# Kernel optimization log

Measured on AMD Instinct MI355X. Metric: run time of the kernel, lower is better.

## Reference

```python
import jax, jax.numpy as jnp
import numpy as np

B, N, F_IN, F_OUT, H = 8, 1024, 128, 64, 4
EPS = 1e-7
NEG_SLOPE = 0.2


def setup_inputs() -> dict:
    key = jax.random.key(0)
    k_a, k_x, k_w, k_aw, k_ab = jax.random.split(key, 5)
    A = jax.random.randint(k_a, (B, N, N), 0, 2).astype(jnp.float32)
    x = jax.random.normal(k_x, (B, N, F_IN), dtype=jnp.float32)
    # per-head params (stacked over head axis): GAT.W (xavier-normal-ish), attention Linear(2F->1)
    W = jax.random.normal(k_w, (H, F_IN, F_OUT), dtype=jnp.float32) * np.sqrt(2.0 / (F_IN + F_OUT))
    lim = 1.0 / np.sqrt(2 * F_OUT)
    a_w = jax.random.uniform(k_aw, (H, 2 * F_OUT), minval=-lim, maxval=lim, dtype=jnp.float32)
    a_b = jax.random.uniform(k_ab, (H,), minval=-lim, maxval=lim, dtype=jnp.float32)
    return {"A": A, "x": x, "W": W, "a_w": a_w, "a_b": a_b}


def reference(A, x, W, a_w, a_b):
    # Wh: (B, H, N, F_OUT)
    Wh = jnp.einsum('bnf,hfo->bhno', x, W)
    # attention linear on concat([Wh_i, Wh_j]) is separable: a1.Wh_i + a2.Wh_j + b
    a1, a2 = a_w[:, :F_OUT], a_w[:, F_OUT:]
    s_i = jnp.einsum('bhno,ho->bhn', Wh, a1)   # depends on row index i (dim 1 of (B,N,N))
    s_j = jnp.einsum('bhno,ho->bhn', Wh, a2)   # depends on col index j (dim 2)
    e = s_i[:, :, :, None] + s_j[:, :, None, :] + a_b[None, :, None, None]  # (B,H,Ni,Nj)
    e = jnp.where(e >= 0, e, NEG_SLOPE * e)  # LeakyReLU(0.2)
    # masked softmax as in source: exp, mask by A, normalize over dim=1 of (B,N,N) -> axis 2 here
    exps = jnp.exp(e) * A[:, None, :, :]
    attn = exps / (jnp.sum(exps, axis=2, keepdims=True) + EPS)
    out = jnp.einsum('bhij,bhjo->bhio', attn, Wh)  # matmul over j
    # concat heads on feature dim: (B, N, H*F_OUT)
    return out.transpose(0, 2, 1, 3).reshape(B, N, H * F_OUT)
```

## Files before the change

kernel.cpp:

```cpp
#include <hip/hip_runtime.h>
#include <hip/hip_bf16.h>
#include <hip/hip_fp16.h>

#define BB 8
#define NN 1024
#define FIN 128
#define FOUT 64
#define HH 4
#define EPSV 1e-7f
#define SLOPE 0.2f
#define LOG2E 1.44269504088896340736f

typedef _Float16 v8h __attribute__((ext_vector_type(8)));
typedef _Float16 v4h __attribute__((ext_vector_type(4)));
typedef _Float16 v2h __attribute__((ext_vector_type(2)));
typedef __fp16 v2hf __attribute__((ext_vector_type(2)));
typedef float v4f __attribute__((ext_vector_type(4)));

union U8 { v2h p[4]; v8h v; };
union U2 { v2hf hf; v2h h; };

__device__ __forceinline__ v2h clamp01(v2h x) {
  v2h zero = {(_Float16)0.0f, (_Float16)0.0f};
  v2h one = {(_Float16)1.0f, (_Float16)1.0f};
  return __builtin_elementwise_min(__builtin_elementwise_max(x, zero), one);
}

__device__ __forceinline__ v2h cvt2(float a, float b) {
  U2 u;
  u.hf = __builtin_amdgcn_cvt_pkrtz(a, b);
  return u.h;
}

__device__ __forceinline__ float dot2(v2h a, v2h b, float c) {
  U2 ua, ub;
  ua.h = a;
  ub.h = b;
  return __builtin_amdgcn_fdot2(ua.hf, ub.hf, c, false);
}

__global__ __launch_bounds__(256) void k0_wt(const float* __restrict__ W,
                                             _Float16* __restrict__ Wtt) {
  for (int it = 0; it < 16; ++it) {
    int idx = blockIdx.x * 4096 + it * 256 + threadIdx.x;
    int e = idx & 7, ln = (idx >> 3) & 15, kgg = (idx >> 7) & 15,
        ct = idx >> 11;
    int c = ct * 16 + ln, k = kgg * 8 + e;
    Wtt[idx] = (_Float16)W[(size_t)(c >> 6) * 8192 + k * 64 + (c & 63)];
  }
}

__global__ __launch_bounds__(256) void k1_whm(
    const float* __restrict__ x, const _Float16* __restrict__ Wtt,
    const float* __restrict__ aw, const float* __restrict__ ab,
    _Float16* __restrict__ WhTt, float* __restrict__ si2,
    _Float16* __restrict__ tjh, _Float16* __restrict__ djh,
    _Float16* __restrict__ e2jh, float* __restrict__ e2i_t,
    float* __restrict__ di_t, float* __restrict__ colsum) {
  __shared__ _Float16 xs[16][136];
  int tid = threadIdx.x;
  int bid = blockIdx.x;
  if (tid < 64) colsum[bid * 64 + tid] = 0.0f;
#pragma unroll
  for (int t2 = 0; t2 < 2; ++t2) {
    int idx = t2 * 256 + tid;
    int row = idx >> 5, c4 = (idx & 31) * 4;
    float4 v = *(const float4*)(x + ((size_t)bid * 16 + row) * FIN + c4);
    v4h hv;
    hv[0] = (_Float16)v.x; hv[1] = (_Float16)v.y;
    hv[2] = (_Float16)v.z; hv[3] = (_Float16)v.w;
    *(v4h*)(&xs[row][c4]) = hv;
  }
  __syncthreads();
  int w = tid >> 6, l = tid & 63;
  int kg = l >> 4, ln = l & 15;
  v4f acc[4] = {{}, {}, {}, {}};
#pragma unroll
  for (int ks = 0; ks < 4; ++ks) {
    v8h af = *(const v8h*)(&xs[ln][ks * 32 + kg * 8]);
    int kgg = ks * 4 + kg;
#pragma unroll
    for (int t = 0; t < 4; ++t) {
      int ct = w * 4 + t;
      v8h bf = *(const v8h*)(Wtt + (((size_t)ct * 16 + kgg) * 16 + ln) * 8);
      acc[t] = __builtin_amdgcn_mfma_f32_16x16x32_f16(af, bf, acc[t], 0, 0, 0);
    }
  }
  float a1v[4], a2v[4];
#pragma unroll
  for (int t = 0; t < 4; ++t) {
    a1v[t] = aw[w * 128 + t * 16 + ln];
    a2v[t] = aw[w * 128 + 64 + t * 16 + ln];
  }
  float abv = ab[w];
#pragma unroll
  for (int r = 0; r < 4; ++r) {
    float v1 = acc[0][r] * a1v[0] + acc[1][r] * a1v[1] +
               acc[2][r] * a1v[2] + acc[3][r] * a1v[3];
    float v2 = acc[0][r] * a2v[0] + acc[1][r] * a2v[1] +
               acc[2][r] * a2v[2] + acc[3][r] * a2v[3];
#pragma unroll
    for (int off = 1; off < 16; off <<= 1) {
      v1 += __shfl_xor(v1, off);
      v2 += __shfl_xor(v2, off);
    }
    if (ln == 0) {
      int gr = bid * 16 + kg * 4 + r;
      int b_ = gr >> 10, n_ = gr & 1023;
      size_t row = ((size_t)b_ * HH + w) * NN + n_;
      float v1L = v1 * LOG2E;
      float tjL = (v2 + abv) * LOG2E;
      si2[row] = v1L;
      float e1i = __builtin_amdgcn_exp2f(v1L);
      float e2i = __builtin_amdgcn_exp2f(0.2f * v1L);
      e2i_t[row] = e2i;
      di_t[row] = e1i - e2i;
      float e1j = __builtin_amdgcn_exp2f(tjL);
      float e2j = __builtin_amdgcn_exp2f(0.2f * tjL);
      tjh[row] = (_Float16)tjL;
      e2jh[row] = (_Float16)e2j;
      djh[row] = (_Float16)(e1j - e2j);
    }
  }
  {
    int b_ = bid >> 6;
    int bh = b_ * HH + w;
    int jb = (bid & 63) >> 1;
    int jj0 = (bid & 1) * 16 + kg * 4;
#pragma unroll
    for (int t = 0; t < 4; ++t) {
      v4h hv;
#pragma unroll
      for (int r = 0; r < 4; ++r) hv[r] = (_Float16)acc[t][r];
      *(v4h*)(WhTt + (((size_t)bh * 32 + jb) * 64 + (t * 16 + ln)) * 32 +
              jj0) = hv;
    }
  }
}

__global__ __launch_bounds__(256) void kb_colsum_bits(
    const float* __restrict__ A, const float* __restrict__ si2,
    const float* __restrict__ e2i_t, const float* __restrict__ di_t,
    const _Float16* __restrict__ tjh, const _Float16* __restrict__ djh,
    const _Float16* __restrict__ e2jh, float* __restrict__ colsum,
    unsigned long long* __restrict__ Abits) {
  __shared__ v2h si_p[4][16], di_p[4][16], e2i_p[4][16];
  int b = blockIdx.z, is = blockIdx.y, jt = blockIdx.x;
  int tid = threadIdx.x;
  int w = tid >> 6, lane = tid & 63;
  int j = jt * 256 + tid;
  int i0 = is * 32;
  if (tid < 64) {
    int h = tid >> 4, pp = tid & 15;
    size_t row = ((size_t)(b * HH + h)) * NN + i0 + 2 * pp;
    si_p[h][pp] = cvt2(si2[row], si2[row + 1]);
    di_p[h][pp] = cvt2(di_t[row], di_t[row + 1]);
    e2i_p[h][pp] = cvt2(e2i_t[row], e2i_t[row + 1]);
  }
  __syncthreads();
  v2h tjb[4], djb[4], ejb[4];
#pragma unroll
  for (int h = 0; h < 4; ++h) {
    size_t jr = ((size_t)(b * HH + h)) * NN + j;
    _Float16 t = tjh[jr], d = djh[jr], e = e2jh[jr];
    tjb[h][0] = t; tjb[h][1] = t;
    djb[h][0] = d; djb[h][1] = d;
    ejb[h][0] = e; ejb[h][1] = e;
  }
  v2h big = {(_Float16)4096.0f, (_Float16)4096.0f};
  float acc[4] = {0.f, 0.f, 0.f, 0.f};
  const float* Ap = A + ((size_t)b * NN + i0) * NN + j;
  unsigned long long myword = 0ull;
#pragma unroll
  for (int c = 0; c < 4; ++c) {
    float av[8];
#pragma unroll
    for (int q = 0; q < 8; ++q) av[q] = Ap[(size_t)(c * 8 + q) * NN];
    v2h apk[4];
#pragma unroll
    for (int q = 0; q < 4; ++q) apk[q] = cvt2(av[2 * q], av[2 * q + 1]);
#pragma unroll
    for (int q = 0; q < 8; ++q) {
      unsigned long long m = __ballot(av[q] != 0.0f);
      if (lane == c * 8 + q) myword = m;
    }
#pragma unroll
    for (int h = 0; h < 4; ++h) {
      U8 si4, di4, ei4;
      si4.v = *(const v8h*)&si_p[h][c * 4];
      di4.v = *(const v8h*)&di_p[h][c * 4];
      ei4.v = *(const v8h*)&e2i_p[h][c * 4];
#pragma unroll
      for (int pp = 0; pp < 4; ++pp) {
        v2h f = si4.p[pp] + tjb[h];
        v2h s = clamp01(f * big);
        v2h ei = s * di4.p[pp] + ei4.p[pp];
        v2h ej = s * djb[h] + ejb[h];
        v2h p = ei * ej;
        acc[h] = dot2(p, apk[pp], acc[h]);
      }
    }
  }
  if (lane < 32)
    Abits[((size_t)b * NN + i0 + lane) * 16 + jt * 4 + w] = myword;
#pragma unroll
  for (int h = 0; h < 4; ++h)
    atomicAdd(&colsum[((size_t)(b * HH + h)) * NN + j], acc[h]);
}

__global__ __launch_bounds__(512, 4) void k4_pv(
    const unsigned long long* __restrict__ Abits,
    const float* __restrict__ si2, const _Float16* __restrict__ tjh,
    const _Float16* __restrict__ djh, const _Float16* __restrict__ e2jh,
    const float* __restrict__ e2i_t, const float* __restrict__ di_t,
    const _Float16* __restrict__ WhTt, const float* __restrict__ colsum,
    float* __restrict__ out) {
  __shared__ unsigned long long Ab[64][17];
  __shared__ _Float16 tjl[2][1024];
  __shared__ _Float16 djl[2][1024];
  __shared__ _Float16 e2jl[2][1024];
  __shared__ _Float16 lut[256][8];
  __shared__ float sil[2][64], e2il[2][64], dil[2][64];
  __shared__ float red[2][2][64][33];
  int bid = blockIdx.x;
  int b = bid & 7, hp = (bid >> 3) & 1, it = bid >> 4;
  int i0 = it * 64;
  int tid = threadIdx.x;
  {
    size_t base = (size_t)(b * HH + hp * 2) * NN;
#pragma unroll
    for (int t2 = 0; t2 < 4; ++t2) {
      int idx = t2 * 512 + tid;
      int hh = idx >> 10, j = idx & 1023;
      size_t row = base + (size_t)hh * NN + j;
      float rr = 1.0f / (colsum[row] + EPSV);
      tjl[hh][j] = tjh[row];
      djl[hh][j] = (_Float16)((float)djh[row] * rr);
      e2jl[hh][j] = (_Float16)((float)e2jh[row] * rr);
    }
  }
  if (tid < 128) {
    int hh = tid >> 6, ii = tid & 63;
    size_t row = (size_t)(b * HH + hp * 2 + hh) * NN + i0 + ii;
    sil[hh][ii] = si2[row];
    e2il[hh][ii] = e2i_t[row];
    dil[hh][ii] = di_t[row];
  }
  if (tid < 256) {
#pragma unroll
    for (int e = 0; e < 8; ++e)
      lut[tid][e] = ((tid >> e) & 1) ? (_Float16)1.0f : (_Float16)0.0f;
  }
  {
#pragma unroll
    for (int t2 = 0; t2 < 2; ++t2) {
      int idx = t2 * 512 + tid;
      int row = idx >> 4, word = idx & 15;
      Ab[row][word] = Abits[((size_t)b * NN + i0 + row) * 16 + word];
    }
  }
  __syncthreads();

  int w = tid >> 6, l = tid & 63;
  int hh = w & 1, jq4 = w >> 1;
  int kg = l >> 4, ln = l & 15;
  v2h si_f[4], e2_f[4], di_f[4];
#pragma unroll
  for (int f = 0; f < 4; ++f) {
    _Float16 s = (_Float16)sil[hh][f * 16 + ln];
    _Float16 e = (_Float16)e2il[hh][f * 16 + ln];
    _Float16 d = (_Float16)dil[hh][f * 16 + ln];
    si_f[f][0] = s; si_f[f][1] = s;
    e2_f[f][0] = e; e2_f[f][1] = e;
    di_f[f][0] = d; di_f[f][1] = d;
  }
  v2h big = {(_Float16)4096.0f, (_Float16)4096.0f};
  int bh = b * HH + hp * 2 + hh;
  v4f acc[4][4] = {};
  const _Float16* VTb = WhTt + (size_t)bh * 32 * 64 * 32;
  int jbase = jq4 * 256;

  for (int jq = 0; jq < 8; ++jq) {
    int j = jbase + jq * 32 + kg * 8;
    int widx = j >> 6, sh = j & 63;
    U8 tj8, dj8, ej8;
    tj8.v = *(const v8h*)&tjl[hh][j];
    dj8.v = *(const v8h*)&djl[hh][j];
    ej8.v = *(const v8h*)&e2jl[hh][j];
    const _Float16* vb = VTb + (size_t)(j >> 5) * 2048 + kg * 8;
    v8h b0 = *(const v8h*)(vb + (0 * 16 + ln) * 32);
    v8h b1 = *(const v8h*)(vb + (1 * 16 + ln) * 32);
    v8h b2 = *(const v8h*)(vb + (2 * 16 + ln) * 32);
    v8h b3 = *(const v8h*)(vb + (3 * 16 + ln) * 32);
#pragma unroll
    for (int f = 0; f < 4; ++f) {
      unsigned int bits = (unsigned int)(Ab[f * 16 + ln][widx] >> sh) & 0xffu;
      U8 m, af;
      m.v = *(const v8h*)&lut[bits][0];
#pragma unroll
      for (int q = 0; q < 4; ++q) {
        v2h fv = tj8.p[q] + si_f[f];
        v2h s = clamp01(fv * big);
        v2h ej = s * dj8.p[q] + ej8.p[q];
        v2h ei = s * di_f[f] + e2_f[f];
        af.p[q] = ei * ej * m.p[q];
      }
      acc[f][0] =
          __builtin_amdgcn_mfma_f32_16x16x32_f16(af.v, b0, acc[f][0], 0, 0, 0);
      acc[f][1] =
          __builtin_amdgcn_mfma_f32_16x16x32_f16(af.v, b1, acc[f][1], 0, 0, 0);
      acc[f][2] =
          __builtin_amdgcn_mfma_f32_16x16x32_f16(af.v, b2, acc[f][2], 0, 0, 0);
      acc[f][3] =
          __builtin_amdgcn_mfma_f32_16x16x32_f16(af.v, b3, acc[f][3], 0, 0, 0);
    }
  }

#pragma unroll
  for (int pass = 0; pass < 2; ++pass) {
    int fA = pass * 2, fB = pass * 2 + 1;
    if (pass) __syncthreads();
    if (jq4 == 1 || jq4 == 3) {
      int slot = jq4 >> 1;
#pragma unroll
      for (int t = 0; t < 4; ++t)
#pragma unroll
        for (int r = 0; r < 4; ++r) {
          red[hh][slot][l][t * 4 + r] = acc[fA][t][r];
          red[hh][slot][l][16 + t * 4 + r] = acc[fB][t][r];
        }
    }
    __syncthreads();
    if (jq4 == 0 || jq4 == 2) {
      int slot = jq4 >> 1;
#pragma unroll
      for (int t = 0; t < 4; ++t)
#pragma unroll
        for (int r = 0; r < 4; ++r) {
          acc[fA][t][r] += red[hh][slot][l][t * 4 + r];
          acc[fB][t][r] += red[hh][slot][l][16 + t * 4 + r];
        }
    }
    __syncthreads();
    if (jq4 == 2) {
#pragma unroll
      for (int t = 0; t < 4; ++t)
#pragma unroll
        for (int r = 0; r < 4; ++r) {
          red[hh][0][l][t * 4 + r] = acc[fA][t][r];
          red[hh][0][l][16 + t * 4 + r] = acc[fB][t][r];
        }
    }
    __syncthreads();
    if (jq4 == 0) {
#pragma unroll
      for (int t = 0; t < 4; ++t)
#pragma unroll
        for (int r = 0; r < 4; ++r) {
          acc[fA][t][r] += red[hh][0][l][t * 4 + r];
          acc[fB][t][r] += red[hh][0][l][16 + t * 4 + r];
        }
#pragma unroll
      for (int r = 0; r < 4; ++r) {
        int giA = i0 + fA * 16 + kg * 4 + r;
        float* opA = out + ((size_t)b * NN + giA) * 256 + (hp * 2 + hh) * 64;
        opA[0 * 16 + ln] = acc[fA][0][r];
        opA[1 * 16 + ln] = acc[fA][1][r];
        opA[2 * 16 + ln] = acc[fA][2][r];
        opA[3 * 16 + ln] = acc[fA][3][r];
        float* opB = opA + 16 * 256;
        opB[0 * 16 + ln] = acc[fB][0][r];
        opB[1 * 16 + ln] = acc[fB][1][r];
        opB[2 * 16 + ln] = acc[fB][2][r];
        opB[3 * 16 + ln] = acc[fB][3][r];
      }
    }
  }
}

extern "C" void kernel_launch(void* const* d_in, const int* in_sizes, int n_in,
                              void* d_out, int out_size, void* d_ws,
                              size_t ws_size, hipStream_t stream) {
  const float* A = (const float*)d_in[0];
  const float* x = (const float*)d_in[1];
  const float* W = (const float*)d_in[2];
  const float* aw = (const float*)d_in[3];
  const float* ab = (const float*)d_in[4];
  float* out = (float*)d_out;
  char* ws = (char*)d_ws;
  _Float16* WhTt = (_Float16*)ws;
  _Float16* Wtt = (_Float16*)(ws + (4u << 20));
  float* si2 = (float*)(ws + (4u << 20) + (64u << 10));
  float* colsum = (float*)(ws + (4u << 20) + (192u << 10));
  unsigned long long* Abits =
      (unsigned long long*)(ws + (4u << 20) + (320u << 10));
  char* tb = ws + (5u << 20) + (320u << 10);
  _Float16* tjh = (_Float16*)tb;
  _Float16* djh = (_Float16*)(tb + (64u << 10));
  _Float16* e2jh = (_Float16*)(tb + (128u << 10));
  float* e2i_t = (float*)(tb + (192u << 10));
  float* di_t = (float*)(tb + (320u << 10));

  hipLaunchKernelGGL(k0_wt, dim3(8), dim3(256), 0, stream, W, Wtt);
  hipLaunchKernelGGL(k1_whm, dim3(512), dim3(256), 0, stream, x, Wtt, aw, ab,
                     WhTt, si2, tjh, djh, e2jh, e2i_t, di_t, colsum);
  hipLaunchKernelGGL(kb_colsum_bits, dim3(4, 32, BB), dim3(256), 0, stream, A,
                     si2, e2i_t, di_t, tjh, djh, e2jh, colsum, Abits);
  hipLaunchKernelGGL(k4_pv, dim3(256), dim3(512), 0, stream, Abits, si2, tjh,
                     djh, e2jh, e2i_t, di_t, WhTt, colsum, out);
}
```

Measured before the change: 41.20 us.

## Fuse weight transpose into projection kernel via per-block LDS staging

Removes the separate k0_wt kernel that converted W to fp16 in an MFMA-tiled layout. Each k1_whm block now loads all of W in fp32, converts it, and scatters it into a 64KB shared-memory buffer. The MFMA B fragments are then read from LDS instead of global memory. This saves one kernel launch and its global round trip. In exchange, all 512 blocks each re-read the full W from cache, do scattered LDS writes, and need about 68KB of LDS per block, which lowers occupancy.

```diff
diff --git a/kernel.cpp b/kernel.cpp
--- a/kernel.cpp
+++ b/kernel.cpp
@@ -39,28 +39,33 @@
   return __builtin_amdgcn_fdot2(ua.hf, ub.hf, c, false);
 }
 
-__global__ __launch_bounds__(256) void k0_wt(const float* __restrict__ W,
-                                             _Float16* __restrict__ Wtt) {
-  for (int it = 0; it < 16; ++it) {
-    int idx = blockIdx.x * 4096 + it * 256 + threadIdx.x;
-    int e = idx & 7, ln = (idx >> 3) & 15, kgg = (idx >> 7) & 15,
-        ct = idx >> 11;
-    int c = ct * 16 + ln, k = kgg * 8 + e;
-    Wtt[idx] = (_Float16)W[(size_t)(c >> 6) * 8192 + k * 64 + (c & 63)];
-  }
-}
-
 __global__ __launch_bounds__(256) void k1_whm(
-    const float* __restrict__ x, const _Float16* __restrict__ Wtt,
+    const float* __restrict__ x, const float* __restrict__ W,
     const float* __restrict__ aw, const float* __restrict__ ab,
     _Float16* __restrict__ WhTt, float* __restrict__ si2,
     _Float16* __restrict__ tjh, _Float16* __restrict__ djh,
     _Float16* __restrict__ e2jh, float* __restrict__ e2i_t,
     float* __restrict__ di_t, float* __restrict__ colsum) {
+  __shared__ _Float16 wlds[32768];
   __shared__ _Float16 xs[16][136];
   int tid = threadIdx.x;
   int bid = blockIdx.x;
   if (tid < 64) colsum[bid * 64 + tid] = 0.0f;
+#pragma unroll 4
+  for (int it = 0; it < 32; ++it) {
+    int idx4 = it * 256 + tid;
+    int base = idx4 * 4;
+    int h = base >> 13, k = (base >> 6) & 127, o0 = base & 63;
+    float4 v = *(const float4*)(W + (size_t)h * 8192 + k * 64 + o0);
+    int kgg = k >> 3, e = k & 7;
+#pragma unroll
+    for (int q = 0; q < 4; ++q) {
+      int c = h * 64 + o0 + q;
+      int ct = c >> 4, ln = c & 15;
+      float val = (q == 0) ? v.x : (q == 1) ? v.y : (q == 2) ? v.z : v.w;
+      wlds[(((ct * 16) + kgg) * 16 + ln) * 8 + e] = (_Float16)val;
+    }
+  }
 #pragma unroll
   for (int t2 = 0; t2 < 2; ++t2) {
     int idx = t2 * 256 + tid;
@@ -82,7 +87,7 @@
 #pragma unroll
     for (int t = 0; t < 4; ++t) {
       int ct = w * 4 + t;
-      v8h bf = *(const v8h*)(Wtt + (((size_t)ct * 16 + kgg) * 16 + ln) * 8);
+      v8h bf = *(const v8h*)(&wlds[(((ct * 16) + kgg) * 16 + ln) * 8]);
       acc[t] = __builtin_amdgcn_mfma_f32_16x16x32_f16(af, bf, acc[t], 0, 0, 0);
     }
   }
@@ -389,20 +394,18 @@
   float* out = (float*)d_out;
   char* ws = (char*)d_ws;
   _Float16* WhTt = (_Float16*)ws;
-  _Float16* Wtt = (_Float16*)(ws + (4u << 20));
-  float* si2 = (float*)(ws + (4u << 20) + (64u << 10));
-  float* colsum = (float*)(ws + (4u << 20) + (192u << 10));
+  float* si2 = (float*)(ws + (4u << 20));
+  float* colsum = (float*)(ws + (4u << 20) + (128u << 10));
   unsigned long long* Abits =
-      (unsigned long long*)(ws + (4u << 20) + (320u << 10));
-  char* tb = ws + (5u << 20) + (320u << 10);
+      (unsigned long long*)(ws + (4u << 20) + (256u << 10));
+  char* tb = ws + (5u << 20) + (256u << 10);
   _Float16* tjh = (_Float16*)tb;
   _Float16* djh = (_Float16*)(tb + (64u << 10));
   _Float16* e2jh = (_Float16*)(tb + (128u << 10));
   float* e2i_t = (float*)(tb + (192u << 10));
   float* di_t = (float*)(tb + (320u << 10));
 
-  hipLaunchKernelGGL(k0_wt, dim3(8), dim3(256), 0, stream, W, Wtt);
-  hipLaunchKernelGGL(k1_whm, dim3(512), dim3(256), 0, stream, x, Wtt, aw, ab,
+  hipLaunchKernelGGL(k1_whm, dim3(512), dim3(256), 0, stream, x, W, aw, ab,
                      WhTt, si2, tjh, djh, e2jh, e2i_t, di_t, colsum);
   hipLaunchKernelGGL(kb_colsum_bits, dim3(4, 32, BB), dim3(256), 0, stream, A,
                      si2, e2i_t, di_t, tjh, djh, e2jh, colsum, Abits);
```

After: 42.69 us. +3.6%, slower.
